# Kernel tuning notes

Measured on AMD Instinct MI355X. Metric: run time of the kernel, lower is better.

## Reference

```python
import jax, jax.numpy as jnp
import numpy as np

N, K = 16384, 16
SIZE, DIST = 256, 64
HEADS, ATTN = 8, 32
HIDDEN = 512
HA = HEADS * ATTN  # 256
EDGE = SIZE + DIST  # key/value input size per edge


def setup_inputs() -> dict:
    key = jax.random.key(0)
    ks = jax.random.split(key, 16)
    s = lambda k, fi, fo: jax.random.normal(k, (fi, fo), jnp.float32) / np.sqrt(fi)
    return {
        "features": jax.random.normal(ks[0], (N, SIZE), jnp.float32),
        "distances": jax.random.normal(ks[1], (N, K, DIST), jnp.float32),
        "structure": jax.random.randint(ks[2], (N, K), 0, N, jnp.int32),
        # local MLP: size -> hidden -> hidden -> size (depth=3 linears)
        "W0": s(ks[3], SIZE, HIDDEN), "b0": jnp.zeros((HIDDEN,), jnp.float32),
        "W1": s(ks[4], HIDDEN, HIDDEN), "b1": jnp.zeros((HIDDEN,), jnp.float32),
        "W2": s(ks[5], HIDDEN, SIZE), "b2": jnp.zeros((SIZE,), jnp.float32),
        # neighbour dot multi-head attention
        "Wq": s(ks[6], SIZE, HA), "bq": jnp.zeros((HA,), jnp.float32),
        "Wk": s(ks[7], EDGE, HA), "bk": jnp.zeros((HA,), jnp.float32),
        "Wv": s(ks[8], EDGE, HA), "bv": jnp.zeros((HA,), jnp.float32),
        "Wo": s(ks[9], HA, SIZE), "bo": jnp.zeros((SIZE,), jnp.float32),
    }


def reference(features, distances, structure,
              W0, b0, W1, b1, W2, b2,
              Wq, bq, Wk, bk, Wv, bv, Wo, bo):
    # batch_norm=False -> bn layers are identity; activation = relu
    inputs = jax.nn.relu(features)                      # [N, size]
    # local MLP (ReLU between layers), then outer activation
    h = jax.nn.relu(inputs @ W0 + b0)
    h = jax.nn.relu(h @ W1 + b1)
    local = jax.nn.relu(h @ W2 + b2)                    # [N, size]
    # edge structure: gather neighbour features, concat distance features
    neigh = local[structure]                            # [N, K, size]
    edge = jnp.concatenate([neigh, distances], axis=-1) # [N, K, size+dist]
    # neighbour-restricted multi-head dot attention
    q = (features @ Wq + bq).reshape(N, HEADS, ATTN)    # [N, H, A]
    k = (edge @ Wk + bk).reshape(N, K, HEADS, ATTN)     # [N, K, H, A]
    v = (edge @ Wv + bv).reshape(N, K, HEADS, ATTN)
    scale = jnp.float32(1.0 / np.sqrt(ATTN))
    scores = jnp.einsum('nha,nkha->nhk', q, k) * scale  # [N, H, K]
    attn = jax.nn.softmax(scores, axis=-1)
    o = jnp.einsum('nhk,nkha->nha', attn, v).reshape(N, HA)
    out = o @ Wo + bo                                   # [N, size]
    return features + out
```

## Files before the change

kernel.cpp:

```cpp
#include <hip/hip_runtime.h>
#include <hip/hip_bf16.h>

#define NN 16384
#define SIZE 256
#define DISTD 64
#define KNBR 16
#define HEADS 8
#define HIDDEN 512
#define HA 256

typedef __bf16 bf16;
typedef bf16 bf16x4 __attribute__((ext_vector_type(4)));
typedef bf16 bf16x8 __attribute__((ext_vector_type(8)));
typedef float f32x4 __attribute__((ext_vector_type(4)));

__device__ __forceinline__ void gload16(const void* g, void* l) {
    __builtin_amdgcn_global_load_lds(
        (const __attribute__((address_space(1))) unsigned int*)g,
        (__attribute__((address_space(3))) unsigned int*)l, 16, 0, 0);
}

template<bool BIAS, bool RELU_OUT, bool RESID, typename OutT>
__global__ __launch_bounds__(256) void gemm128(
    const bf16* __restrict__ A, const bf16* __restrict__ BT,
    const float* __restrict__ bias, const float* __restrict__ resid,
    OutT* __restrict__ C, int M, int N, int K)
{
    __shared__ alignas(16) bf16 As[2][128][32];
    __shared__ alignas(16) bf16 Bs[2][128][32];

    const int t = threadIdx.x;
    const int w = t >> 6, l = t & 63;
    const int bm = blockIdx.y * 128, bn = blockIdx.x * 128;
    const int wr = (w >> 1) * 64, wc = (w & 1) * 64;

    f32x4 acc[4][4] = {};

    const bf16* ag = A  + (size_t)(bm + (t >> 2)) * K + (t & 3) * 8;
    const bf16* bg = BT + (size_t)(bn + (t >> 2)) * K + (t & 3) * 8;

    const int nt = K >> 5;

    {
        bf16* asl = &As[0][w << 4][0];
        bf16* bsl = &Bs[0][w << 4][0];
        gload16(ag, asl);
        gload16(ag + (size_t)64 * K, (char*)asl + 4096);
        gload16(bg, bsl);
        gload16(bg + (size_t)64 * K, (char*)bsl + 4096);
    }
    __syncthreads();

    for (int tt = 0; tt < nt; ++tt) {
        const int cur = tt & 1;
        if (tt + 1 < nt) {
            const int k0 = (tt + 1) << 5;
            bf16* asl = &As[cur ^ 1][w << 4][0];
            bf16* bsl = &Bs[cur ^ 1][w << 4][0];
            gload16(ag + k0, asl);
            gload16(ag + k0 + (size_t)64 * K, (char*)asl + 4096);
            gload16(bg + k0, bsl);
            gload16(bg + k0 + (size_t)64 * K, (char*)bsl + 4096);
        }

        bf16x8 af[4], bfr[4];
        #pragma unroll
        for (int m = 0; m < 4; ++m)
            af[m] = *(const bf16x8*)&As[cur][wr + m * 16 + (l & 15)][(l >> 4) * 8];
        #pragma unroll
        for (int n2 = 0; n2 < 4; ++n2)
            bfr[n2] = *(const bf16x8*)&Bs[cur][wc + n2 * 16 + (l & 15)][(l >> 4) * 8];
        #pragma unroll
        for (int m = 0; m < 4; ++m)
            #pragma unroll
            for (int n2 = 0; n2 < 4; ++n2)
                acc[m][n2] = __builtin_amdgcn_mfma_f32_16x16x32_bf16(
                    af[m], bfr[n2], acc[m][n2], 0, 0, 0);

        __syncthreads();
    }

    #pragma unroll
    for (int m = 0; m < 4; ++m) {
        const int row = bm + wr + m * 16 + ((l >> 4) << 2);
        #pragma unroll
        for (int n2 = 0; n2 < 4; ++n2) {
            const int col = bn + wc + n2 * 16 + (l & 15);
            #pragma unroll
            for (int i = 0; i < 4; ++i) {
                float v = acc[m][n2][i];
                if (BIAS) v += bias[col];
                if (RESID) v += resid[(size_t)(row + i) * N + col];
                if (RELU_OUT) v = fmaxf(v, 0.f);
                C[(size_t)(row + i) * N + col] = (OutT)v;
            }
        }
    }
}

__global__ __launch_bounds__(256) void feat2bf(const float4* __restrict__ f,
                                               bf16x4* __restrict__ fbf,
                                               bf16x4* __restrict__ frbf)
{
    int id = blockIdx.x * 256 + threadIdx.x;
    float4 v = f[id];
    bf16x4 a, r;
    a[0] = (bf16)v.x; a[1] = (bf16)v.y; a[2] = (bf16)v.z; a[3] = (bf16)v.w;
    r[0] = (bf16)fmaxf(v.x, 0.f); r[1] = (bf16)fmaxf(v.y, 0.f);
    r[2] = (bf16)fmaxf(v.z, 0.f); r[3] = (bf16)fmaxf(v.w, 0.f);
    fbf[id] = a; frbf[id] = r;
}

__global__ __launch_bounds__(256) void prep_weights(
    const float* __restrict__ W0, const float* __restrict__ W1,
    const float* __restrict__ W2, const float* __restrict__ Wq,
    const float* __restrict__ bq, const float* __restrict__ Wk,
    const float* __restrict__ Wv, const float* __restrict__ Wo,
    const float* __restrict__ bo, const float* __restrict__ bv,
    bf16* __restrict__ W0T, bf16* __restrict__ W1T, bf16* __restrict__ W2T,
    bf16* __restrict__ WkvT, bf16* __restrict__ WqcatT, bf16* __restrict__ WstackT,
    float* __restrict__ bqcat, float* __restrict__ biaso)
{
    long id = blockIdx.x * 256L + threadIdx.x;
    if (id < 131072) {
        int n = id >> 8, k = id & 255;
        W0T[id] = (bf16)W0[(long)k * 512 + n]; return;
    }
    id -= 131072;
    if (id < 262144) {
        int n = id >> 9, k = id & 511;
        W1T[id] = (bf16)W1[(long)k * 512 + n]; return;
    }
    id -= 262144;
    if (id < 131072) {
        int n = id >> 9, k = id & 511;
        W2T[id] = (bf16)W2[(long)k * 256 + n]; return;
    }
    id -= 131072;
    if (id < 131072) {
        int n = id >> 8, k = id & 255;
        WkvT[id] = (bf16)(n < 256 ? Wk[(long)k * 256 + n] : Wv[(long)k * 256 + (n - 256)]);
        return;
    }
    id -= 131072;
    if (id < 196608) {
        int col = id >> 8, c = id & 255;
        float s;
        if (col < 256) s = Wq[(long)c * 256 + col];
        else {
            int hd = col - 256, h = hd >> 6, d = hd & 63;
            s = 0.f;
            #pragma unroll
            for (int a = 0; a < 32; ++a)
                s += Wq[(long)c * 256 + h * 32 + a] * Wk[(long)(256 + d) * 256 + h * 32 + a];
        }
        WqcatT[id] = (bf16)s; return;
    }
    id -= 196608;
    if (id < 196608) {
        int col = (int)(id / 768), r = (int)(id % 768);
        float s;
        if (r < 256) s = Wo[(long)r * 256 + col];
        else {
            int hd = r - 256, h = hd >> 6, d = hd & 63;
            s = 0.f;
            #pragma unroll
            for (int a = 0; a < 32; ++a)
                s += Wv[(long)(256 + d) * 256 + h * 32 + a] * Wo[(long)(h * 32 + a) * 256 + col];
        }
        WstackT[id] = (bf16)s; return;
    }
    id -= 196608;
    if (id < 768) {
        float s;
        if (id < 256) s = bq[id];
        else {
            int hd = (int)id - 256, h = hd >> 6, d = hd & 63;
            s = 0.f;
            #pragma unroll
            for (int a = 0; a < 32; ++a)
                s += bq[h * 32 + a] * Wk[(long)(256 + d) * 256 + h * 32 + a];
        }
        bqcat[id] = s; return;
    }
    id -= 768;
    if (id < 256) {
        float s = bo[id];
        for (int u = 0; u < 256; ++u) s += bv[u] * Wo[(long)u * 256 + id];
        biaso[id] = s;
    }
}

__global__ __launch_bounds__(256) void attn_kernel(
    const bf16* __restrict__ qcat,
    const bf16* __restrict__ localKV,
    const float* __restrict__ dist,
    const int*  __restrict__ structure,
    bf16* __restrict__ concat)
{
    const int n = blockIdx.x;
    const int t = threadIdx.x;
    const int h = t >> 5, j = (t >> 1) & 15, part = t & 1;

    __shared__ float dist_s[16][65];
    __shared__ bf16  V_s[16][264];
    __shared__ float attn_s[8][16];
    __shared__ int   s_s[16];

    {
        const float* dp = dist + (long)n * (KNBR * DISTD);
        #pragma unroll
        for (int i = 0; i < 4; ++i) {
            int e = i * 256 + t;
            dist_s[e >> 6][e & 63] = dp[e];
        }
    }
    if (t < 16) s_s[t] = structure[(long)n * KNBR + t];
    __syncthreads();

    #pragma unroll
    for (int pass = 0; pass < 2; ++pass) {
        int idx = pass * 256 + t;
        int row = idx >> 5, chunk = idx & 31;
        bf16x8 v = *(const bf16x8*)(localKV + (long)s_s[row] * 512 + 256 + chunk * 8);
        *(bf16x8*)&V_s[row][chunk * 8] = v;
    }

    const bf16* qp_q = qcat + (long)n * 768 + h * 32 + part * 16;
    bf16x8 qa = *(const bf16x8*)qp_q;
    bf16x8 qb = *(const bf16x8*)(qp_q + 8);
    const bf16* qp_p = qcat + (long)n * 768 + 256 + h * 64 + part * 32;
    bf16x8 p0 = *(const bf16x8*)qp_p;
    bf16x8 p1 = *(const bf16x8*)(qp_p + 8);
    bf16x8 p2 = *(const bf16x8*)(qp_p + 16);
    bf16x8 p3 = *(const bf16x8*)(qp_p + 24);
    const bf16* kp = localKV + (long)s_s[j] * 512 + h * 32 + part * 16;
    bf16x8 ka = *(const bf16x8*)kp;
    bf16x8 kb = *(const bf16x8*)(kp + 8);

    float sc = 0.f;
    #pragma unroll
    for (int i = 0; i < 8; ++i)
        sc += (float)qa[i] * (float)ka[i] + (float)qb[i] * (float)kb[i];

    const int dbase = part * 32;
    #pragma unroll
    for (int i = 0; i < 8; ++i) sc += dist_s[j][dbase + i]      * (float)p0[i];
    #pragma unroll
    for (int i = 0; i < 8; ++i) sc += dist_s[j][dbase + 8 + i]  * (float)p1[i];
    #pragma unroll
    for (int i = 0; i < 8; ++i) sc += dist_s[j][dbase + 16 + i] * (float)p2[i];
    #pragma unroll
    for (int i = 0; i < 8; ++i) sc += dist_s[j][dbase + 24 + i] * (float)p3[i];

    sc += __shfl_xor(sc, 1);
    float s = sc * 0.17677669529663687f;
    float m = s;
    m = fmaxf(m, __shfl_xor(m, 2));
    m = fmaxf(m, __shfl_xor(m, 4));
    m = fmaxf(m, __shfl_xor(m, 8));
    m = fmaxf(m, __shfl_xor(m, 16));
    float e = __expf(s - m);
    float sum = e;
    sum += __shfl_xor(sum, 2);
    sum += __shfl_xor(sum, 4);
    sum += __shfl_xor(sum, 8);
    sum += __shfl_xor(sum, 16);
    float attn = e / sum;
    if (!part) attn_s[h][j] = attn;
    __syncthreads();

    float acc = 0.f;
    #pragma unroll
    for (int j2 = 0; j2 < 16; ++j2)
        acc += attn_s[h][j2] * (float)V_s[j2][t];
    concat[(long)n * 768 + t] = (bf16)acc;

    #pragma unroll
    for (int rep = 0; rep < 2; ++rep) {
        int idx = rep * 256 + t;
        int h3 = idx >> 6, d3 = idx & 63;
        float s2 = 0.f;
        #pragma unroll
        for (int j2 = 0; j2 < 16; ++j2)
            s2 += attn_s[h3][j2] * dist_s[j2][d3];
        concat[(long)n * 768 + 256 + idx] = (bf16)s2;
    }
}

extern "C" void kernel_launch(void* const* d_in, const int* in_sizes, int n_in,
                              void* d_out, int out_size, void* d_ws, size_t ws_size,
                              hipStream_t stream)
{
    const float* features = (const float*)d_in[0];
    const float* dist     = (const float*)d_in[1];
    const int*   structure= (const int*)d_in[2];
    const float* W0 = (const float*)d_in[3];
    const float* b0 = (const float*)d_in[4];
    const float* W1 = (const float*)d_in[5];
    const float* b1 = (const float*)d_in[6];
    const float* W2 = (const float*)d_in[7];
    const float* b2 = (const float*)d_in[8];
    const float* Wq = (const float*)d_in[9];
    const float* bq = (const float*)d_in[10];
    const float* Wk = (const float*)d_in[11];
    const float* Wv = (const float*)d_in[13];
    const float* bv = (const float*)d_in[14];
    const float* Wo = (const float*)d_in[15];
    const float* bo = (const float*)d_in[16];
    float* out = (float*)d_out;

    const size_t MB = 1u << 20;
    char* w = (char*)d_ws;
    bf16*  fbf     = (bf16*)(w + 0 * MB);
    bf16*  frbf    = (bf16*)(w + 8 * MB);
    bf16*  local_b = (bf16*)(w + 8 * MB);
    bf16*  H0      = (bf16*)(w + 16 * MB);
    bf16*  qcat    = (bf16*)(w + 16 * MB);
    bf16*  H1      = (bf16*)(w + 32 * MB);
    bf16*  localKV = (bf16*)(w + 40 * MB);
    bf16*  concat  = (bf16*)(w + 56 * MB);
    char*  wb      = w + 80 * MB;
    bf16*  W0T     = (bf16*)(wb + 0);
    bf16*  W1T     = (bf16*)(wb + 262144);
    bf16*  W2T     = (bf16*)(wb + 786432);
    bf16*  WkvT    = (bf16*)(wb + 1048576);
    bf16*  WqcatT  = (bf16*)(wb + 1310720);
    bf16*  WstackT = (bf16*)(wb + 1703936);
    float* bqcat   = (float*)(wb + 2097152);
    float* biaso   = (float*)(wb + 2100224);

    dim3 blk(256);

    feat2bf<<<dim3(4096), blk, 0, stream>>>((const float4*)features, (bf16x4*)fbf, (bf16x4*)frbf);
    prep_weights<<<dim3(4100), blk, 0, stream>>>(
        W0, W1, W2, Wq, bq, Wk, Wv, Wo, bo, bv,
        W0T, W1T, W2T, WkvT, WqcatT, WstackT, bqcat, biaso);

    gemm128<true,  true,  false, bf16><<<dim3(4, 128), blk, 0, stream>>>(
        frbf, W0T, b0, nullptr, H0, NN, 512, 256);
    gemm128<true,  true,  false, bf16><<<dim3(4, 128), blk, 0, stream>>>(
        H0, W1T, b1, nullptr, H1, NN, 512, 512);
    gemm128<true,  true,  false, bf16><<<dim3(2, 128), blk, 0, stream>>>(
        H1, W2T, b2, nullptr, local_b, NN, 256, 512);

    gemm128<true,  false, false, bf16><<<dim3(6, 128), blk, 0, stream>>>(
        fbf, WqcatT, bqcat, nullptr, qcat, NN, 768, 256);

    gemm128<false, false, false, bf16><<<dim3(4, 128), blk, 0, stream>>>(
        local_b, WkvT, nullptr, nullptr, localKV, NN, 512, 256);

    attn_kernel<<<dim3(NN), blk, 0, stream>>>(qcat, localKV, dist, structure, concat);

    gemm128<true,  false, true,  float><<<dim3(2, 128), blk, 0, stream>>>(
        concat, WstackT, biaso, features, out, NN, 256, 768);
}
```

Baseline: 168.5 us.

## Fuse prep kernels and first GEMM with query GEMM, restructure attention epilogue

Merges the feature conversion into the weight-prep kernel and runs the first MLP GEMM and the query-concat GEMM as one grid, cutting launches and filling more CUs per launch. The attention scale is folded into the query weights and bias. The distance-projected query part is now stored in fp32 instead of bf16, which doubles that buffer's traffic but keeps more precision. The attention output phase is rewritten with vectorised shared-memory reads split across thread halves, and the dist_s row padding changes to allow 16-byte loads.

```diff
diff --git a/kernel.cpp b/kernel.cpp
--- a/kernel.cpp
+++ b/kernel.cpp
@@ -8,8 +8,10 @@
 #define HEADS 8
 #define HIDDEN 512
 #define HA 256
+#define SCALE 0.17677669529663687f
 
 typedef __bf16 bf16;
+typedef bf16 bf16x2 __attribute__((ext_vector_type(2)));
 typedef bf16 bf16x4 __attribute__((ext_vector_type(4)));
 typedef bf16 bf16x8 __attribute__((ext_vector_type(8)));
 typedef float f32x4 __attribute__((ext_vector_type(4)));
@@ -40,7 +42,6 @@
     const bf16* bg = BT + (size_t)(bn + (t >> 2)) * K + (t & 3) * 8;
 
     const int nt = K >> 5;
-
     {
         bf16* asl = &As[0][w << 4][0];
         bf16* bsl = &Bs[0][w << 4][0];
@@ -62,7 +63,6 @@
             gload16(bg + k0, bsl);
             gload16(bg + k0 + (size_t)64 * K, (char*)bsl + 4096);
         }
-
         bf16x8 af[4], bfr[4];
         #pragma unroll
         for (int m = 0; m < 4; ++m)
@@ -76,7 +76,6 @@
             for (int n2 = 0; n2 < 4; ++n2)
                 acc[m][n2] = __builtin_amdgcn_mfma_f32_16x16x32_bf16(
                     af[m], bfr[n2], acc[m][n2], 0, 0, 0);
-
         __syncthreads();
     }
 
@@ -98,30 +97,116 @@
     }
 }
 
-__global__ __launch_bounds__(256) void feat2bf(const float4* __restrict__ f,
-                                               bf16x4* __restrict__ fbf,
-                                               bf16x4* __restrict__ frbf)
+__global__ __launch_bounds__(256) void g1qcat_kernel(
+    const bf16* __restrict__ fbf, const bf16* __restrict__ frbf,
+    const bf16* __restrict__ W0T, const float* __restrict__ b0,
+    const bf16* __restrict__ WqcatT, const float* __restrict__ bqcat,
+    bf16* __restrict__ H0, bf16* __restrict__ qbf, float* __restrict__ qprojF)
 {
-    int id = blockIdx.x * 256 + threadIdx.x;
-    float4 v = f[id];
-    bf16x4 a, r;
-    a[0] = (bf16)v.x; a[1] = (bf16)v.y; a[2] = (bf16)v.z; a[3] = (bf16)v.w;
-    r[0] = (bf16)fmaxf(v.x, 0.f); r[1] = (bf16)fmaxf(v.y, 0.f);
-    r[2] = (bf16)fmaxf(v.z, 0.f); r[3] = (bf16)fmaxf(v.w, 0.f);
-    fbf[id] = a; frbf[id] = r;
-}
-
-__global__ __launch_bounds__(256) void prep_weights(
+    __shared__ alignas(16) bf16 As[2][128][32];
+    __shared__ alignas(16) bf16 Bs[2][128][32];
+
+    const int bx = blockIdx.x, by = blockIdx.y;
+    const bool isG1 = bx < 4;
+    const int cx = bx - 4;
+    const bf16* A  = isG1 ? frbf : fbf;
+    const bf16* BT = isG1 ? (W0T + (size_t)bx * 128 * 256)
+                          : (WqcatT + (size_t)cx * 128 * 256);
+    const float* bias = isG1 ? (b0 + bx * 128) : (bqcat + cx * 128);
+    const int K = 256;
+
+    const int t = threadIdx.x;
+    const int w = t >> 6, l = t & 63;
+    const int bm = by * 128;
+    const int wr = (w >> 1) * 64, wc = (w & 1) * 64;
+
+    f32x4 acc[4][4] = {};
+
+    const bf16* ag = A  + (size_t)(bm + (t >> 2)) * K + (t & 3) * 8;
+    const bf16* bg = BT + (size_t)(t >> 2) * K + (t & 3) * 8;
+
+    {
+        bf16* asl = &As[0][w << 4][0];
+        bf16* bsl = &Bs[0][w << 4][0];
+        gload16(ag, asl);
+        gload16(ag + (size_t)64 * K, (char*)asl + 4096);
+        gload16(bg, bsl);
+        gload16(bg + (size_t)64 * K, (char*)bsl + 4096);
+    }
+    __syncthreads();
+
+    for (int tt = 0; tt < 8; ++tt) {
+        const int cur = tt & 1;
+        if (tt + 1 < 8) {
+            const int k0 = (tt + 1) << 5;
+            bf16* asl = &As[cur ^ 1][w << 4][0];
+            bf16* bsl = &Bs[cur ^ 1][w << 4][0];
+            gload16(ag + k0, asl);
+            gload16(ag + k0 + (size_t)64 * K, (char*)asl + 4096);
+            gload16(bg + k0, bsl);
+            gload16(bg + k0 + (size_t)64 * K, (char*)bsl + 4096);
+        }
+        bf16x8 af[4], bfr[4];
+        #pragma unroll
+        for (int m = 0; m < 4; ++m)
+            af[m] = *(const bf16x8*)&As[cur][wr + m * 16 + (l & 15)][(l >> 4) * 8];
+        #pragma unroll
+        for (int n2 = 0; n2 < 4; ++n2)
+            bfr[n2] = *(const bf16x8*)&Bs[cur][wc + n2 * 16 + (l & 15)][(l >> 4) * 8];
+        #pragma unroll
+        for (int m = 0; m < 4; ++m)
+            #pragma unroll
+            for (int n2 = 0; n2 < 4; ++n2)
+                acc[m][n2] = __builtin_amdgcn_mfma_f32_16x16x32_bf16(
+                    af[m], bfr[n2], acc[m][n2], 0, 0, 0);
+        __syncthreads();
+    }
+
+    #pragma unroll
+    for (int m = 0; m < 4; ++m) {
+        const int lrow = wr + m * 16 + ((l >> 4) << 2);
+        #pragma unroll
+        for (int n2 = 0; n2 < 4; ++n2) {
+            const int lcol = wc + n2 * 16 + (l & 15);
+            #pragma unroll
+            for (int i = 0; i < 4; ++i) {
+                float v = acc[m][n2][i] + bias[lcol];
+                const size_t row = bm + lrow + i;
+                if (isG1) {
+                    H0[row * 512 + bx * 128 + lcol] = (bf16)fmaxf(v, 0.f);
+                } else if (cx < 2) {
+                    qbf[row * 256 + cx * 128 + lcol] = (bf16)v;
+                } else {
+                    qprojF[row * 512 + (cx - 2) * 128 + lcol] = v;
+                }
+            }
+        }
+    }
+}
+
+__global__ __launch_bounds__(256) void prep_all(
+    const float* __restrict__ features,
     const float* __restrict__ W0, const float* __restrict__ W1,
     const float* __restrict__ W2, const float* __restrict__ Wq,
     const float* __restrict__ bq, const float* __restrict__ Wk,
     const float* __restrict__ Wv, const float* __restrict__ Wo,
     const float* __restrict__ bo, const float* __restrict__ bv,
+    bf16* __restrict__ fbf, bf16* __restrict__ frbf,
     bf16* __restrict__ W0T, bf16* __restrict__ W1T, bf16* __restrict__ W2T,
     bf16* __restrict__ WkvT, bf16* __restrict__ WqcatT, bf16* __restrict__ WstackT,
     float* __restrict__ bqcat, float* __restrict__ biaso)
 {
-    long id = blockIdx.x * 256L + threadIdx.x;
+    if (blockIdx.x < 4096) {
+        int id = blockIdx.x * 256 + threadIdx.x;
+        float4 v = ((const float4*)features)[id];
+        bf16x4 a, r;
+        a[0] = (bf16)v.x; a[1] = (bf16)v.y; a[2] = (bf16)v.z; a[3] = (bf16)v.w;
+        r[0] = (bf16)fmaxf(v.x, 0.f); r[1] = (bf16)fmaxf(v.y, 0.f);
+        r[2] = (bf16)fmaxf(v.z, 0.f); r[3] = (bf16)fmaxf(v.w, 0.f);
+        ((bf16x4*)fbf)[id] = a; ((bf16x4*)frbf)[id] = r;
+        return;
+    }
+    long id = (blockIdx.x - 4096) * 256L + threadIdx.x;
     if (id < 131072) {
         int n = id >> 8, k = id & 255;
         W0T[id] = (bf16)W0[(long)k * 512 + n]; return;
@@ -154,7 +239,7 @@
             for (int a = 0; a < 32; ++a)
                 s += Wq[(long)c * 256 + h * 32 + a] * Wk[(long)(256 + d) * 256 + h * 32 + a];
         }
-        WqcatT[id] = (bf16)s; return;
+        WqcatT[id] = (bf16)(s * SCALE); return;
     }
     id -= 196608;
     if (id < 196608) {
@@ -181,7 +266,7 @@
             for (int a = 0; a < 32; ++a)
                 s += bq[h * 32 + a] * Wk[(long)(256 + d) * 256 + h * 32 + a];
         }
-        bqcat[id] = s; return;
+        bqcat[id] = s * SCALE; return;
     }
     id -= 768;
     if (id < 256) {
@@ -192,17 +277,18 @@
 }
 
 __global__ __launch_bounds__(256) void attn_kernel(
-    const bf16* __restrict__ qcat,
-    const bf16* __restrict__ localKV,
+    const bf16*  __restrict__ qbf,
+    const float* __restrict__ qprojF,
+    const bf16*  __restrict__ localKV,
     const float* __restrict__ dist,
-    const int*  __restrict__ structure,
+    const int*   __restrict__ structure,
     bf16* __restrict__ concat)
 {
     const int n = blockIdx.x;
     const int t = threadIdx.x;
     const int h = t >> 5, j = (t >> 1) & 15, part = t & 1;
 
-    __shared__ float dist_s[16][65];
+    __shared__ float dist_s[16][68];
     __shared__ bf16  V_s[16][264];
     __shared__ float attn_s[8][16];
     __shared__ int   s_s[16];
@@ -226,14 +312,14 @@
         *(bf16x8*)&V_s[row][chunk * 8] = v;
     }
 
-    const bf16* qp_q = qcat + (long)n * 768 + h * 32 + part * 16;
-    bf16x8 qa = *(const bf16x8*)qp_q;
-    bf16x8 qb = *(const bf16x8*)(qp_q + 8);
-    const bf16* qp_p = qcat + (long)n * 768 + 256 + h * 64 + part * 32;
-    bf16x8 p0 = *(const bf16x8*)qp_p;
-    bf16x8 p1 = *(const bf16x8*)(qp_p + 8);
-    bf16x8 p2 = *(const bf16x8*)(qp_p + 16);
-    bf16x8 p3 = *(const bf16x8*)(qp_p + 24);
+    const bf16* qq = qbf + (long)n * 256 + h * 32 + part * 16;
+    bf16x8 qa = *(const bf16x8*)qq;
+    bf16x8 qb = *(const bf16x8*)(qq + 8);
+    const float* qpp = qprojF + (long)n * 512 + h * 64 + part * 32;
+    float4 qp4[8];
+    #pragma unroll
+    for (int i = 0; i < 8; ++i) qp4[i] = ((const float4*)qpp)[i];
+
     const bf16* kp = localKV + (long)s_s[j] * 512 + h * 32 + part * 16;
     bf16x8 ka = *(const bf16x8*)kp;
     bf16x8 kb = *(const bf16x8*)(kp + 8);
@@ -245,22 +331,20 @@
 
     const int dbase = part * 32;
     #pragma unroll
-    for (int i = 0; i < 8; ++i) sc += dist_s[j][dbase + i]      * (float)p0[i];
-    #pragma unroll
-    for (int i = 0; i < 8; ++i) sc += dist_s[j][dbase + 8 + i]  * (float)p1[i];
-    #pragma unroll
-    for (int i = 0; i < 8; ++i) sc += dist_s[j][dbase + 16 + i] * (float)p2[i];
-    #pragma unroll
-    for (int i = 0; i < 8; ++i) sc += dist_s[j][dbase + 24 + i] * (float)p3[i];
+    for (int i = 0; i < 8; ++i) {
+        sc += dist_s[j][dbase + 4 * i + 0] * qp4[i].x;
+        sc += dist_s[j][dbase + 4 * i + 1] * qp4[i].y;
+        sc += dist_s[j][dbase + 4 * i + 2] * qp4[i].z;
+        sc += dist_s[j][dbase + 4 * i + 3] * qp4[i].w;
+    }
 
     sc += __shfl_xor(sc, 1);
-    float s = sc * 0.17677669529663687f;
-    float m = s;
+    float m = sc;
     m = fmaxf(m, __shfl_xor(m, 2));
     m = fmaxf(m, __shfl_xor(m, 4));
     m = fmaxf(m, __shfl_xor(m, 8));
     m = fmaxf(m, __shfl_xor(m, 16));
-    float e = __expf(s - m);
+    float e = __expf(sc - m);
     float sum = e;
     sum += __shfl_xor(sum, 2);
     sum += __shfl_xor(sum, 4);
@@ -270,21 +354,34 @@
     if (!part) attn_s[h][j] = attn;
     __syncthreads();
 
-    float acc = 0.f;
-    #pragma unroll
-    for (int j2 = 0; j2 < 16; ++j2)
-        acc += attn_s[h][j2] * (float)V_s[j2][t];
-    concat[(long)n * 768 + t] = (bf16)acc;
-
-    #pragma unroll
-    for (int rep = 0; rep < 2; ++rep) {
-        int idx = rep * 256 + t;
-        int h3 = idx >> 6, d3 = idx & 63;
-        float s2 = 0.f;
-        #pragma unroll
-        for (int j2 = 0; j2 < 16; ++j2)
-            s2 += attn_s[h3][j2] * dist_s[j2][d3];
-        concat[(long)n * 768 + 256 + idx] = (bf16)s2;
+    if (t < 128) {
+        const int c0 = t * 2;
+        const int hh = t >> 4;
+        float a0 = 0.f, a1 = 0.f;
+        #pragma unroll
+        for (int j2 = 0; j2 < 16; ++j2) {
+            float wgt = attn_s[hh][j2];
+            bf16x2 pv = *(const bf16x2*)&V_s[j2][c0];
+            a0 += wgt * (float)pv[0];
+            a1 += wgt * (float)pv[1];
+        }
+        bf16x2 o2; o2[0] = (bf16)a0; o2[1] = (bf16)a1;
+        *(bf16x2*)&concat[(long)n * 768 + c0] = o2;
+    } else {
+        const int u = t - 128;
+        const int base = u * 4;
+        const int h3 = u >> 4, d3 = (u & 15) * 4;
+        f32x4 acc4 = {};
+        #pragma unroll
+        for (int j2 = 0; j2 < 16; ++j2) {
+            float wgt = attn_s[h3][j2];
+            const f32x4 dv = *(const f32x4*)&dist_s[j2][d3];
+            acc4 += wgt * dv;
+        }
+        bf16x4 o4;
+        #pragma unroll
+        for (int i = 0; i < 4; ++i) o4[i] = (bf16)acc4[i];
+        *(bf16x4*)&concat[(long)n * 768 + 256 + base] = o4;
     }
 }
 
@@ -312,15 +409,16 @@
 
     const size_t MB = 1u << 20;
     char* w = (char*)d_ws;
-    bf16*  fbf     = (bf16*)(w + 0 * MB);
-    bf16*  frbf    = (bf16*)(w + 8 * MB);
-    bf16*  local_b = (bf16*)(w + 8 * MB);
-    bf16*  H0      = (bf16*)(w + 16 * MB);
-    bf16*  qcat    = (bf16*)(w + 16 * MB);
-    bf16*  H1      = (bf16*)(w + 32 * MB);
-    bf16*  localKV = (bf16*)(w + 40 * MB);
-    bf16*  concat  = (bf16*)(w + 56 * MB);
-    char*  wb      = w + 80 * MB;
+    float* qprojF  = (float*)(w + 0 * MB);
+    bf16*  qbf     = (bf16*)(w + 32 * MB);
+    bf16*  H0      = (bf16*)(w + 40 * MB);
+    bf16*  local_b = (bf16*)(w + 40 * MB);
+    bf16*  concat  = (bf16*)(w + 48 * MB);
+    bf16*  fbf     = (bf16*)(w + 56 * MB);
+    bf16*  frbf    = (bf16*)(w + 64 * MB);
+    bf16*  H1      = (bf16*)(w + 56 * MB);
+    bf16*  localKV = (bf16*)(w + 72 * MB);
+    char*  wb      = w + 88 * MB;
     bf16*  W0T     = (bf16*)(wb + 0);
     bf16*  W1T     = (bf16*)(wb + 262144);
     bf16*  W2T     = (bf16*)(wb + 786432);
@@ -332,25 +430,23 @@
 
     dim3 blk(256);
 
-    feat2bf<<<dim3(4096), blk, 0, stream>>>((const float4*)features, (bf16x4*)fbf, (bf16x4*)frbf);
-    prep_weights<<<dim3(4100), blk, 0, stream>>>(
-        W0, W1, W2, Wq, bq, Wk, Wv, Wo, bo, bv,
-        W0T, W1T, W2T, WkvT, WqcatT, WstackT, bqcat, biaso);
-
-    gemm128<true,  true,  false, bf16><<<dim3(4, 128), blk, 0, stream>>>(
-        frbf, W0T, b0, nullptr, H0, NN, 512, 256);
+    prep_all<<<dim3(8196), blk, 0, stream>>>(
+        features, W0, W1, W2, Wq, bq, Wk, Wv, Wo, bo, bv,
+        fbf, frbf, W0T, W1T, W2T, WkvT, WqcatT, WstackT, bqcat, biaso);
+
+    g1qcat_kernel<<<dim3(10, 128), blk, 0, stream>>>(
+        fbf, frbf, W0T, b0, WqcatT, bqcat, H0, qbf, qprojF);
+
     gemm128<true,  true,  false, bf16><<<dim3(4, 128), blk, 0, stream>>>(
         H0, W1T, b1, nullptr, H1, NN, 512, 512);
     gemm128<true,  true,  false, bf16><<<dim3(2, 128), blk, 0, stream>>>(
         H1, W2T, b2, nullptr, local_b, NN, 256, 512);
 
-    gemm128<true,  false, false, bf16><<<dim3(6, 128), blk, 0, stream>>>(
-        fbf, WqcatT, bqcat, nullptr, qcat, NN, 768, 256);
-
     gemm128<false, false, false, bf16><<<dim3(4, 128), blk, 0, stream>>>(
         local_b, WkvT, nullptr, nullptr, localKV, NN, 512, 256);
 
-    attn_kernel<<<dim3(NN), blk, 0, stream>>>(qcat, localKV, dist, structure, concat);
+    attn_kernel<<<dim3(NN), blk, 0, stream>>>(
+        qbf, qprojF, localKV, dist, structure, concat);
 
     gemm128<true,  false, true,  float><<<dim3(2, 128), blk, 0, stream>>>(
         concat, WstackT, biaso, features, out, NN, 256, 768);
```

New measurement: 180.0 us. +6.8%, slower.
